# Performance work log

Measured on AMD Instinct MI355X. Metric: run time of the kernel, lower is better.

## Reference

```python
import jax, jax.numpy as jnp
import numpy as np

B, L, D, K_F = 2, 1024, 768, 16  # batch, seq_len, n_embd, num_eigh**2
N_FFT = 2048


def setup_inputs() -> dict:
    key = jax.random.key(0)
    k1, k2, k3, k4 = jax.random.split(key, 4)
    x = jax.random.normal(k1, (B, L, D), dtype=jnp.float32)
    phi = jax.random.normal(k2, (L, K_F), dtype=jnp.float32) * 0.1
    M_phi_plus = jax.random.normal(k3, (K_F, D, D), dtype=jnp.float32) * (1.0 / np.sqrt(K_F * D))
    M_phi_minus = jax.random.normal(k4, (K_F, D, D), dtype=jnp.float32) * (1.0 / np.sqrt(K_F * D))
    return {"x": x, "phi": phi, "M_phi_plus": M_phi_plus, "M_phi_minus": M_phi_minus, "n": N_FFT}


def _convolve(u, v, n):
    """FFT causal convolution with K spectral filters (flash-stu `convolve`, use_approx=False).
    u: [B, L, D] inputs; v: [L, K] filters; n: FFT length (>= 2L-1 padded pow2).
    Returns U_plus, U_minus: [B, L, K, D].
    """
    b, l, d = u.shape
    sgn = jnp.where(jnp.arange(l) % 2 == 0, 1.0, -1.0).astype(u.dtype)  # alternating +/-
    # Stack the plain and sign-modulated signals: [B, L, 1, D, 2]
    U = jnp.stack([u, u * sgn[None, :, None]], axis=-1)[:, :, None, :, :]
    Uf = jnp.fft.rfft(U, n=n, axis=1)                      # [B, F, 1, D, 2] complex
    vf = jnp.fft.rfft(v, n=n, axis=0)[None, :, :, None, None]  # [1, F, K, 1, 1]
    conv = jnp.fft.irfft(vf * Uf, n=n, axis=1)[:, :l]      # [B, L, K, D, 2]
    U_plus = conv[..., 0]
    U_minus = conv[..., 1] * sgn[None, :, None, None]
    return U_plus, U_minus


def reference(x, phi, M_phi_plus, M_phi_minus, n):
    U_plus, U_minus = _convolve(x, phi, n)
    # tensordot(U, M, dims=([2,3],[0,2])): contract eigenmode k and input channel i
    spectral_plus = jnp.einsum('blki,koi->blo', U_plus, M_phi_plus)
    spectral_minus = jnp.einsum('blki,koi->blo', U_minus, M_phi_minus)
    return spectral_plus + spectral_minus
```

## Files before the change

kernel.cpp:

```cpp
#include <hip/hip_runtime.h>
#include <hip/hip_fp16.h>

typedef unsigned short u16;
typedef unsigned int   u32;
typedef _Float16 f16;
typedef __attribute__((ext_vector_type(8))) f16 f16x8;
typedef __attribute__((ext_vector_type(2))) __fp16 fp16x2;
typedef __attribute__((ext_vector_type(4))) float f32x4;

#define B_SZ  2
#define L_SEQ 1024
#define D_EMB 768
#define KF    16
#define MDIM  (B_SZ * L_SEQ)
#define KROW  (KF * D_EMB)
#define MELEM ((size_t)KF * D_EMB * D_EMB)
#define NTILE 96
#define PT_SZ 16384

__device__ __forceinline__ void gload16(const void* g, void* l) {
    __builtin_amdgcn_global_load_lds(
        (const __attribute__((address_space(1))) u32*)g,
        (__attribute__((address_space(3))) u32*)l, 16, 0, 0);
}

__global__ __launch_bounds__(256) void stu_setup(const float* __restrict__ x,
                                                 const float* __restrict__ phi,
                                                 u16* __restrict__ xT,
                                                 u16* __restrict__ Ttab) {
    __shared__ __align__(16) float xs[64][68];
    const int bid = blockIdx.x;
    const int tid = threadIdx.x;

    if (bid < 384) {
        const int s0 = (bid & 15) << 6;
        const int d0 = ((bid >> 4) % 12) << 6;
        const int b  = bid / 192;

#pragma unroll
        for (int j = 0; j < 4; ++j) {
            int c = tid + (j << 8);
            int row = c >> 4;
            int col = (c & 15) << 2;
            *(float4*)&xs[row][col] =
                *(const float4*)&x[((size_t)b * L_SEQ + s0 + row) * D_EMB + d0 + col];
        }
        __syncthreads();

        const int dl = tid >> 2;
        const int ss = (tid & 3) << 4;
        const int dg = d0 + dl;
        const int xorv = (dg & 7) << 3;

        union { u16 v[16]; uint4 q[2]; } pk;
#pragma unroll
        for (int u = 0; u < 16; ++u)
            pk.v[u] = __half_as_ushort(__float2half(xs[ss + u][dl]));

        size_t base = (size_t)b * D_EMB * L_SEQ + (size_t)dg * L_SEQ + s0;
        *(uint4*)&xT[base + ( ss      ^ xorv)] = pk.q[0];
        *(uint4*)&xT[base + ((ss + 8) ^ xorv)] = pk.q[1];
    } else {
        const int f = bid - 384;
        const int q = f & 15;
        const int k = f >> 4;
        const int tt  = tid >> 2;
        const int ss0 = (tid & 3) << 4;

        union { u16 v[16]; uint4 q4[2]; } pk;
#pragma unroll
        for (int u = 0; u < 16; ++u) {
            int s = (q << 6) + tt - (ss0 + u);
            float v = (s >= 0 && s < L_SEQ) ? phi[s * KF + k] : 0.f;
            pk.v[u] = __half_as_ushort(__float2half(v));
        }
        u16* tile = Ttab + (((size_t)k * 16 + q) << 12);
        *(uint4*)&tile[(tt << 6) + ss0]     = pk.q4[0];
        *(uint4*)&tile[(tt << 6) + ss0 + 8] = pk.q4[1];
    }
}

__global__ __launch_bounds__(256, 3) void stu_conv_mcvt(
        const u16* __restrict__ xT, const u16* __restrict__ Ttab,
        u16* __restrict__ Up, u16* __restrict__ Um,
        const float* __restrict__ Mp, const float* __restrict__ Mm,
        u16* __restrict__ Hp, u16* __restrict__ Hm) {
    __shared__ __align__(16) u16 Xs[2][192 * 64];

    const int bid = blockIdx.x;
    const int tid = threadIdx.x;

    if (bid < 512) {
        const size_t n8 = MELEM / 8;
        size_t i = (size_t)bid * 256 + tid;
        const size_t stride = (size_t)512 * 256;
        for (size_t cc = i; cc < n8; cc += stride) {
            const size_t g = cc << 3;
            {
                const float4 a0 = *(const float4*)&Mp[g];
                const float4 a1 = *(const float4*)&Mp[g + 4];
                union { fp16x2 h2[4]; uint4 q; } u;
                u.h2[0] = __builtin_amdgcn_cvt_pkrtz(a0.x, a0.y);
                u.h2[1] = __builtin_amdgcn_cvt_pkrtz(a0.z, a0.w);
                u.h2[2] = __builtin_amdgcn_cvt_pkrtz(a1.x, a1.y);
                u.h2[3] = __builtin_amdgcn_cvt_pkrtz(a1.z, a1.w);
                *(uint4*)&Hp[g] = u.q;
            }
            {
                const float4 a0 = *(const float4*)&Mm[g];
                const float4 a1 = *(const float4*)&Mm[g + 4];
                union { fp16x2 h2[4]; uint4 q; } u;
                u.h2[0] = __builtin_amdgcn_cvt_pkrtz(a0.x, a0.y);
                u.h2[1] = __builtin_amdgcn_cvt_pkrtz(a0.z, a0.w);
                u.h2[2] = __builtin_amdgcn_cvt_pkrtz(a1.x, a1.y);
                u.h2[3] = __builtin_amdgcn_cvt_pkrtz(a1.z, a1.w);
                *(uint4*)&Hm[g] = u.q;
            }
        }
        return;
    }

    const int c    = bid - 512;
    const int xcd  = c & 7;
    const int w    = c >> 3;
    const int ti   = 15 - (w >> 4);
    const int t0   = ti << 6;
    const int inner = w & 15;
    const int bk   = (xcd << 2) + (inner >> 2);
    const int b    = bk >> 4;
    const int k    = bk & 15;
    const int d0   = (inner & 3) * 192;

    const int lane = tid & 63;
    const int wid  = tid >> 6;
    const int wr   = wid >> 1;
    const int wc   = wid & 1;
    const int lr   = lane & 15;
    const int lk   = lane >> 4;

    const u32 xm = (lr & 1) ? 0x00008000u : 0x80000000u;

    f32x4 acc[2][2][6];
#pragma unroll
    for (int s = 0; s < 2; ++s)
#pragma unroll
        for (int m = 0; m < 2; ++m)
#pragma unroll
            for (int n = 0; n < 6; ++n)
                acc[s][m][n] = (f32x4){0.f, 0.f, 0.f, 0.f};

    const u16* xTb = xT + (size_t)b * D_EMB * L_SEQ + (size_t)d0 * L_SEQ;
    const u16* Tk  = Ttab + ((size_t)k << 16);

    auto stageX = [&](int buf, int r0) {
#pragma unroll
        for (int j = 0; j < 6; ++j) {
            int cc = tid + (j << 8);
            gload16(xTb + (size_t)(cc >> 3) * L_SEQ + r0 + ((cc & 7) << 3),
                    &Xs[buf][cc << 3]);
        }
    };

    stageX(0, 0);
    __syncthreads();

    int cur = 0;
    for (int r0 = 0; r0 <= t0; r0 += 64) {
        if (r0 < t0) stageX(cur ^ 1, r0 + 64);

        const u16* TpT = Tk + ((size_t)((t0 - r0) >> 6) << 12);
        f16x8 afp[2][2];
#pragma unroll
        for (int m = 0; m < 2; ++m) {
            const int rowt = (wr << 5) + (m << 4) + lr;
#pragma unroll
            for (int kk = 0; kk < 2; ++kk)
                afp[m][kk] = *(const f16x8*)&TpT[(rowt << 6) + (kk << 5) + (lk << 3)];
        }

        const char* XsC = (const char*)&Xs[cur][0];
#pragma unroll
        for (int kk = 0; kk < 2; ++kk) {
            f16x8 bfr[6];
#pragma unroll
            for (int n = 0; n < 6; ++n) {
                const int row = wc * 96 + (n << 4) + lr;
                const int boff = ((kk << 6) + (lk << 4)) ^ ((row & 7) << 4);
                bfr[n] = *(const f16x8*)(XsC + row * 128 + boff);
            }
#pragma unroll
            for (int m = 0; m < 2; ++m) {
                const f16x8 ap = afp[m][kk];
                union { f16x8 h; u32 wv[4]; } cv;
                cv.h = ap;
#pragma unroll
                for (int qd = 0; qd < 4; ++qd) cv.wv[qd] ^= xm;
                const f16x8 am = cv.h;
#pragma unroll
                for (int n = 0; n < 6; ++n) {
                    acc[0][m][n] = __builtin_amdgcn_mfma_f32_16x16x32_f16(
                        ap, bfr[n], acc[0][m][n], 0, 0, 0);
                    acc[1][m][n] = __builtin_amdgcn_mfma_f32_16x16x32_f16(
                        am, bfr[n], acc[1][m][n], 0, 0, 0);
                }
            }
        }
        __syncthreads();
        cur ^= 1;
    }

#pragma unroll
    for (int m = 0; m < 2; ++m) {
        const int trow = t0 + (wr << 5) + (m << 4) + (lk << 2);
#pragma unroll
        for (int n = 0; n < 6; ++n) {
            const int col = d0 + wc * 96 + (n << 4) + lr;
#pragma unroll
            for (int j = 0; j < 4; ++j) {
                size_t idx = ((size_t)(b * L_SEQ + trow + j) * KF + k) * D_EMB + col;
                Up[idx] = __half_as_ushort(__float2half(acc[0][m][n][j]));
                Um[idx] = __half_as_ushort(__float2half(acc[1][m][n][j]));
            }
        }
    }
}

__global__ __launch_bounds__(256) void stu_spectral_mfma(
        const u16* __restrict__ Up, const u16* __restrict__ Um,
        const u16* __restrict__ Mhp, const u16* __restrict__ Mhm,
        float* __restrict__ out, u16* __restrict__ P, int usePartial) {
    __shared__ __align__(16) u16 As[128 * 64];
    __shared__ __align__(16) u16 Bs[128 * 64];

    const int h   = blockIdx.x;
    const int z   = h & 7;
    const int rem = h >> 3;
    const int o0  = (rem % 6) << 7;
    const int m0  = (rem / 6) << 7;
    const int sign = z & 1;
    const int k0 = (z >> 1) << 2;

    const u16* A    = sign ? Um : Up;
    const u16* Bsrc = sign ? Mhm : Mhp;

    const int tid  = threadIdx.x;
    const int lane = tid & 63;
    const int wid  = tid >> 6;
    const int wr   = wid >> 1;
    const int wc   = wid & 1;
    const int lr   = lane & 15;
    const int lk   = lane >> 4;

    f32x4 acc[4][4];
#pragma unroll
    for (int m = 0; m < 4; ++m)
#pragma unroll
        for (int n = 0; n < 4; ++n)
            acc[m][n] = (f32x4){0.f, 0.f, 0.f, 0.f};

    for (int k = k0; k < k0 + 4; ++k) {
        const u16* Ak = A + (size_t)m0 * KROW + k * D_EMB;
        const u16* Bk = Bsrc + (size_t)k * D_EMB * D_EMB + (size_t)o0 * D_EMB;

        for (int ic = 0; ic < D_EMB; ic += 64) {
            __syncthreads();
#pragma unroll
            for (int j = 0; j < 4; ++j) {
                const int c = tid + (j << 8);
                const int row = c >> 3;
                const int off = ((c & 7) ^ (row & 7)) << 3;
                gload16(Ak + (size_t)row * KROW + ic + off, &As[c << 3]);
                gload16(Bk + (size_t)row * D_EMB + ic + off, &Bs[c << 3]);
            }
            __syncthreads();

#pragma unroll
            for (int kk = 0; kk < 2; ++kk) {
                f16x8 af[4], bf[4];
#pragma unroll
                for (int m = 0; m < 4; ++m) {
                    const int row = wr * 64 + (m << 4) + lr;
                    const int boff = (((kk << 2) + lk) ^ (row & 7)) << 4;
                    af[m] = *(const f16x8*)((const char*)&As[0] + row * 128 + boff);
                }
#pragma unroll
                for (int n = 0; n < 4; ++n) {
                    const int row = wc * 64 + (n << 4) + lr;
                    const int boff = (((kk << 2) + lk) ^ (row & 7)) << 4;
                    bf[n] = *(const f16x8*)((const char*)&Bs[0] + row * 128 + boff);
                }
#pragma unroll
                for (int m = 0; m < 4; ++m)
#pragma unroll
                    for (int n = 0; n < 4; ++n)
                        acc[m][n] = __builtin_amdgcn_mfma_f32_16x16x32_f16(
                            af[m], bf[n], acc[m][n], 0, 0, 0);
            }
        }
    }

    if (usePartial) {
        u16* Pt = P + (size_t)h * PT_SZ;
#pragma unroll
        for (int m = 0; m < 4; ++m) {
            const int rowl = wr * 64 + (m << 4) + (lk << 2);
#pragma unroll
            for (int n = 0; n < 4; ++n) {
                const int coll = wc * 64 + (n << 4) + lr;
#pragma unroll
                for (int j = 0; j < 4; ++j)
                    Pt[(rowl + j) * 128 + coll] =
                        __half_as_ushort(__float2half(acc[m][n][j]));
            }
        }
    } else {
#pragma unroll
        for (int m = 0; m < 4; ++m) {
            const int row = m0 + wr * 64 + (m << 4) + (lk << 2);
#pragma unroll
            for (int n = 0; n < 4; ++n) {
                const int col = o0 + wc * 64 + (n << 4) + lr;
#pragma unroll
                for (int j = 0; j < 4; ++j)
                    atomicAdd(&out[(size_t)(row + j) * D_EMB + col], acc[m][n][j]);
            }
        }
    }
}

__global__ __launch_bounds__(256) void stu_reduce(const u16* __restrict__ P,
                                                  float* __restrict__ out) {
    const size_t total = (size_t)MDIM * D_EMB;
    size_t idx = (size_t)blockIdx.x * 256 + threadIdx.x;
    const size_t stride = (size_t)gridDim.x * 256;
    for (; idx < total; idx += stride) {
        const int row = (int)(idx / D_EMB);
        const int col = (int)(idx % D_EMB);
        const int tile = (row >> 7) * 6 + (col >> 7);
        const u16* p = P + (size_t)tile * 8 * PT_SZ + ((row & 127) << 7) + (col & 127);
        float s = 0.f;
#pragma unroll
        for (int z = 0; z < 8; ++z)
            s += __half2float(__ushort_as_half(p[z * PT_SZ]));
        out[idx] = s;
    }
}

extern "C" void kernel_launch(void* const* d_in, const int* in_sizes, int n_in,
                              void* d_out, int out_size, void* d_ws, size_t ws_size,
                              hipStream_t stream) {
    const float* x   = (const float*)d_in[0];
    const float* phi = (const float*)d_in[1];
    const float* Mp  = (const float*)d_in[2];
    const float* Mm  = (const float*)d_in[3];
    float* out = (float*)d_out;

    const size_t S = (size_t)MDIM * KROW;
    u16* Up   = (u16*)d_ws;
    u16* Um   = Up + S;
    u16* Mhp  = Um + S;
    u16* Mhm  = Mhp + MELEM;
    u16* xT   = Mhm + MELEM;
    u16* Ttab = xT + (size_t)B_SZ * D_EMB * L_SEQ;
    u16* Part = Ttab + (size_t)KF * 16 * 4096;

    const size_t elems_needed = 2 * S + 2 * MELEM + 1572864 + 1048576 + 12582912;
    const int usePartial = (ws_size >= elems_needed * sizeof(u16)) ? 1 : 0;

    if (!usePartial)
        (void)hipMemsetAsync(d_out, 0, (size_t)out_size * sizeof(float), stream);

    stu_setup<<<dim3(640), dim3(256), 0, stream>>>(x, phi, xT, Ttab);

    stu_conv_mcvt<<<dim3(2560), dim3(256), 0, stream>>>(
        xT, Ttab, Up, Um, Mp, Mm, Mhp, Mhm);

    stu_spectral_mfma<<<dim3(NTILE * 8), dim3(256), 0, stream>>>(
        Up, Um, Mhp, Mhm, out, Part, usePartial);

    if (usePartial)
        stu_reduce<<<dim3(1536), dim3(256), 0, stream>>>(Part, out);
}
```

Before: 173.6 us.

## Double-buffer spectral GEMM LDS tiles and prefetch Toeplitz fragments in conv kernel

The spectral contraction kernel now double-buffers its A/B LDS tiles. It flattens the k/ic loops into a single 48-iteration loop that issues the next tile's global-to-LDS loads before computing the current one, which cuts one barrier per step. The convolution kernel register-prefetches the next Toeplitz filter fragments alongside the X staging, so global load latency overlaps the MFMA work. The cost is twice the LDS in the spectral kernel (64KB), which may reduce occupancy, plus extra registers in the conv kernel.

```diff
diff --git a/kernel.cpp b/kernel.cpp
--- a/kernel.cpp
+++ b/kernel.cpp
@@ -161,21 +161,30 @@
         }
     };
 
+    const int rowtA = ((wr << 5) + lr) << 6;
+    const int rowtB = ((wr << 5) + 16 + lr) << 6;
+
+    f16x8 tc[2][2], tn[2][2];
+    {
+        const u16* TpT = Tk + ((size_t)ti << 12);
+        tc[0][0] = *(const f16x8*)&TpT[rowtA + (lk << 3)];
+        tc[0][1] = *(const f16x8*)&TpT[rowtA + 32 + (lk << 3)];
+        tc[1][0] = *(const f16x8*)&TpT[rowtB + (lk << 3)];
+        tc[1][1] = *(const f16x8*)&TpT[rowtB + 32 + (lk << 3)];
+    }
     stageX(0, 0);
     __syncthreads();
 
     int cur = 0;
     for (int r0 = 0; r0 <= t0; r0 += 64) {
-        if (r0 < t0) stageX(cur ^ 1, r0 + 64);
-
-        const u16* TpT = Tk + ((size_t)((t0 - r0) >> 6) << 12);
-        f16x8 afp[2][2];
-#pragma unroll
-        for (int m = 0; m < 2; ++m) {
-            const int rowt = (wr << 5) + (m << 4) + lr;
-#pragma unroll
-            for (int kk = 0; kk < 2; ++kk)
-                afp[m][kk] = *(const f16x8*)&TpT[(rowt << 6) + (kk << 5) + (lk << 3)];
+        if (r0 < t0) {
+            const int qn = ((t0 - r0) >> 6) - 1;
+            const u16* TpT = Tk + ((size_t)qn << 12);
+            tn[0][0] = *(const f16x8*)&TpT[rowtA + (lk << 3)];
+            tn[0][1] = *(const f16x8*)&TpT[rowtA + 32 + (lk << 3)];
+            tn[1][0] = *(const f16x8*)&TpT[rowtB + (lk << 3)];
+            tn[1][1] = *(const f16x8*)&TpT[rowtB + 32 + (lk << 3)];
+            stageX(cur ^ 1, r0 + 64);
         }
 
         const char* XsC = (const char*)&Xs[cur][0];
@@ -190,7 +199,7 @@
             }
 #pragma unroll
             for (int m = 0; m < 2; ++m) {
-                const f16x8 ap = afp[m][kk];
+                const f16x8 ap = tc[m][kk];
                 union { f16x8 h; u32 wv[4]; } cv;
                 cv.h = ap;
 #pragma unroll
@@ -206,6 +215,8 @@
             }
         }
         __syncthreads();
+        tc[0][0] = tn[0][0]; tc[0][1] = tn[0][1];
+        tc[1][0] = tn[1][0]; tc[1][1] = tn[1][1];
         cur ^= 1;
     }
 
@@ -229,8 +240,8 @@
         const u16* __restrict__ Up, const u16* __restrict__ Um,
         const u16* __restrict__ Mhp, const u16* __restrict__ Mhm,
         float* __restrict__ out, u16* __restrict__ P, int usePartial) {
-    __shared__ __align__(16) u16 As[128 * 64];
-    __shared__ __align__(16) u16 Bs[128 * 64];
+    __shared__ __align__(16) u16 As[2][128 * 64];
+    __shared__ __align__(16) u16 Bs[2][128 * 64];
 
     const int h   = blockIdx.x;
     const int z   = h & 7;
@@ -258,45 +269,54 @@
         for (int n = 0; n < 4; ++n)
             acc[m][n] = (f32x4){0.f, 0.f, 0.f, 0.f};
 
-    for (int k = k0; k < k0 + 4; ++k) {
-        const u16* Ak = A + (size_t)m0 * KROW + k * D_EMB;
-        const u16* Bk = Bsrc + (size_t)k * D_EMB * D_EMB + (size_t)o0 * D_EMB;
-
-        for (int ic = 0; ic < D_EMB; ic += 64) {
-            __syncthreads();
-#pragma unroll
-            for (int j = 0; j < 4; ++j) {
-                const int c = tid + (j << 8);
-                const int row = c >> 3;
-                const int off = ((c & 7) ^ (row & 7)) << 3;
-                gload16(Ak + (size_t)row * KROW + ic + off, &As[c << 3]);
-                gload16(Bk + (size_t)row * D_EMB + ic + off, &Bs[c << 3]);
-            }
-            __syncthreads();
-
-#pragma unroll
-            for (int kk = 0; kk < 2; ++kk) {
-                f16x8 af[4], bf[4];
-#pragma unroll
-                for (int m = 0; m < 4; ++m) {
-                    const int row = wr * 64 + (m << 4) + lr;
-                    const int boff = (((kk << 2) + lk) ^ (row & 7)) << 4;
-                    af[m] = *(const f16x8*)((const char*)&As[0] + row * 128 + boff);
-                }
-#pragma unroll
-                for (int n = 0; n < 4; ++n) {
-                    const int row = wc * 64 + (n << 4) + lr;
-                    const int boff = (((kk << 2) + lk) ^ (row & 7)) << 4;
-                    bf[n] = *(const f16x8*)((const char*)&Bs[0] + row * 128 + boff);
-                }
-#pragma unroll
-                for (int m = 0; m < 4; ++m)
-#pragma unroll
-                    for (int n = 0; n < 4; ++n)
-                        acc[m][n] = __builtin_amdgcn_mfma_f32_16x16x32_f16(
-                            af[m], bf[n], acc[m][n], 0, 0, 0);
-            }
-        }
+    auto stage = [&](int buf, int it) {
+        const int k  = k0 + it / 12;
+        const int ic = (it % 12) << 6;
+        const u16* Ak = A + (size_t)m0 * KROW + k * D_EMB + ic;
+        const u16* Bk = Bsrc + ((size_t)k * D_EMB + o0) * D_EMB + ic;
+#pragma unroll
+        for (int j = 0; j < 4; ++j) {
+            const int cch = tid + (j << 8);
+            const int row = cch >> 3;
+            const int off = ((cch & 7) ^ (row & 7)) << 3;
+            gload16(Ak + (size_t)row * KROW + off, &As[buf][cch << 3]);
+            gload16(Bk + (size_t)row * D_EMB + off, &Bs[buf][cch << 3]);
+        }
+    };
+
+    stage(0, 0);
+    __syncthreads();
+
+    int cur = 0;
+    for (int it = 0; it < 48; ++it) {
+        if (it < 47) stage(cur ^ 1, it + 1);
+
+        const char* AsC = (const char*)&As[cur][0];
+        const char* BsC = (const char*)&Bs[cur][0];
+#pragma unroll
+        for (int kk = 0; kk < 2; ++kk) {
+            f16x8 af[4], bf[4];
+#pragma unroll
+            for (int m = 0; m < 4; ++m) {
+                const int row = wr * 64 + (m << 4) + lr;
+                const int boff = (((kk << 2) + lk) ^ (row & 7)) << 4;
+                af[m] = *(const f16x8*)(AsC + row * 128 + boff);
+            }
+#pragma unroll
+            for (int n = 0; n < 4; ++n) {
+                const int row = wc * 64 + (n << 4) + lr;
+                const int boff = (((kk << 2) + lk) ^ (row & 7)) << 4;
+                bf[n] = *(const f16x8*)(BsC + row * 128 + boff);
+            }
+#pragma unroll
+            for (int m = 0; m < 4; ++m)
+#pragma unroll
+                for (int n = 0; n < 4; ++n)
+                    acc[m][n] = __builtin_amdgcn_mfma_f32_16x16x32_f16(
+                        af[m], bf[n], acc[m][n], 0, 0, 0);
+        }
+        __syncthreads();
+        cur ^= 1;
     }
 
     if (usePartial) {
```

After: 240.1 us. +38.3%, slower.
